# Kernel tuning notes

Measured on AMD Instinct MI355X. Metric: run time of the kernel, lower is better.

The kernel has to match this reference:

```python
import jax, jax.numpy as jnp
import numpy as np

BATCH = 8
N_CLASSES = 3            # including background
PRE_NMS_LIMIT = 6000
NMS_THRESH = 0.5
SCALE = 512.0
WINDOW = (0.0, 0.0, 512.0, 512.0)   # y1, x1, y2, x2
STD_DEV = np.array([0.1, 0.1, 0.2, 0.2], np.float32)
GROUP_OFFSET = 4096.0    # > image extent; separates (batch, class) groups in NMS

_RATIOS = np.array([0.5, 1.0, 2.0])
_LEVELS = [((128, 128), 4, 8.0), ((64, 64), 8, 16.0), ((32, 32), 16, 32.0), ((16, 16), 32, 64.0)]


def _gen_anchors():
    # faithful port of generate_pyramid_anchors / generate_anchors (anchor_stride=1)
    out = []
    for (fy, fx), stride, scale in _LEVELS:
        s, r = np.meshgrid(np.array([scale]), _RATIOS)
        s, r = s.flatten(), r.flatten()
        heights = s / np.sqrt(r)
        widths = s * np.sqrt(r)
        sy = np.arange(fy) * stride
        sx = np.arange(fx) * stride
        sx, sy = np.meshgrid(sx, sy)
        bw, bcx = np.meshgrid(widths, sx)
        bh, bcy = np.meshgrid(heights, sy)
        centers = np.stack([bcy, bcx], axis=2).reshape(-1, 2)
        sizes = np.stack([bh, bw], axis=2).reshape(-1, 2)
        out.append(np.concatenate([centers - 0.5 * sizes, centers + 0.5 * sizes], axis=1))
    return np.concatenate(out, axis=0).astype(np.float32)  # (65280, 4) yxyx


def setup_inputs() -> dict:
    key = jax.random.key(0)
    k1, k2 = jax.random.split(key)
    anchors = jnp.asarray(_gen_anchors())
    n_anchors = anchors.shape[0]
    n_prop = BATCH * n_anchors
    logits = jax.random.normal(k1, (n_prop, N_CLASSES), jnp.float32)
    probs = jax.nn.softmax(logits, axis=-1)
    deltas = jax.random.normal(k2, (n_prop, 4), jnp.float32)
    batch_ixs = jnp.repeat(jnp.arange(BATCH, dtype=jnp.int64), n_anchors)
    return {"probs": probs, "deltas": deltas, "anchors": anchors, "batch_ixs": batch_ixs}


def _apply_box_deltas_2d(boxes, deltas):
    # boxes: (K,4) yxyx (normalized); deltas: (K,4) dy,dx,dh,dw
    h = boxes[:, 2] - boxes[:, 0]
    w = boxes[:, 3] - boxes[:, 1]
    cy = boxes[:, 0] + 0.5 * h + deltas[:, 0] * h
    cx = boxes[:, 1] + 0.5 * w + deltas[:, 1] * w
    h = h * jnp.exp(deltas[:, 2])
    w = w * jnp.exp(deltas[:, 3])
    y1 = cy - 0.5 * h
    x1 = cx - 0.5 * w
    return jnp.stack([y1, x1, y1 + h, x1 + w], axis=1)


def _nms_keep(boxes, thresh):
    # boxes (K,4), already sorted by score descending; returns bool keep mask.
    y1, x1, y2, x2 = boxes[:, 0], boxes[:, 1], boxes[:, 2], boxes[:, 3]
    areas = (y2 - y1 + 1.0) * (x2 - x1 + 1.0)
    ih = jnp.clip(jnp.minimum(y2[:, None], y2[None, :]) - jnp.maximum(y1[:, None], y1[None, :]) + 1.0, 0.0)
    iw = jnp.clip(jnp.minimum(x2[:, None], x2[None, :]) - jnp.maximum(x1[:, None], x1[None, :]) + 1.0, 0.0)
    inter = ih * iw
    iou = inter / (areas[:, None] + areas[None, :] - inter)  # (K,K)
    K = boxes.shape[0]
    idx = jnp.arange(K)

    def body(i, keep):
        sup = (iou[i] >= thresh) & (idx > i) & keep[i]
        return keep & ~sup

    return jax.lax.fori_loop(0, K, body, jnp.ones((K,), bool))


def reference(probs, deltas, anchors, batch_ixs):
    n_anchors = anchors.shape[0]
    n_fg = probs.shape[1] - 1
    # trim to top pre_nms_limit foreground scores (flat over proposals x fg classes)
    fg = probs[:, 1:].reshape(-1)
    scores, flat_ix = jax.lax.top_k(fg, PRE_NMS_LIMIT)  # sorted descending
    prop_ix = flat_ix // n_fg
    class_ids = flat_ix % n_fg + 1
    b = batch_ixs[prop_ix]
    a = anchors[prop_ix % n_anchors]        # anchors tiled per batch element
    d = deltas[prop_ix] * jnp.asarray(STD_DEV)
    rois = _apply_box_deltas_2d(a / SCALE, d) * SCALE
    lo = jnp.array([WINDOW[0], WINDOW[1], WINDOW[0], WINDOW[1]], rois.dtype)
    hi = jnp.array([WINDOW[2], WINDOW[3], WINDOW[2], WINDOW[3]], rois.dtype)
    rois = jnp.clip(rois, lo, hi)
    # batched per-class NMS: offset boxes so different (batch, class) groups never overlap
    group = (b * (n_fg + 1) + class_ids).astype(rois.dtype) * GROUP_OFFSET
    keep = _nms_keep(rois + group[:, None], NMS_THRESH)
    detections = jnp.concatenate(
        [rois, scores[:, None], keep.astype(rois.dtype)[:, None]], axis=1)  # (K, 6)
    return detections, class_ids, b
```

## Files before the change

kernel.cpp:

```cpp
#include <hip/hip_runtime.h>
#include <math.h>

typedef unsigned int u32;
typedef unsigned short u16;
typedef unsigned long long u64;

#define PRE_NMS 6000
#define NBLK    94
#define KMAX    640
#define MSTRIDE 11
#define MAXW    10
#define MTILE   (MAXW * MAXW)
#define FINEB   8192
#define LOWB    8064
#define TOTB    (FINEB + LOWB)
#define NHB     32
#define CANDMAX 16384
#define NGRP    24
#define FLOOR_BITS 0x3F000000u

#define CTR_OFF    0
#define CAND_OFF   256
#define BOXR_OFF   131328
#define GBITS_OFF  227584
#define KG_OFF     246016
#define GRANKG_OFF 246272
#define BOXG_OFF   307712
#define AREAG_OFF  553472
#define MASKG_OFF  614912
#define BASE_OFF   1966592
#define BCNT_OFF   2032128
#define PART_OFF   2097664

__device__ __forceinline__ u32 bucket_of(u32 bits) {
    if (bits >= FLOOR_BITS) {
        u32 fb = (bits - FLOOR_BITS) >> 10; if (fb > FINEB - 1) fb = FINEB - 1;
        return fb;
    }
    return 8192u + (bits >> 17);
}

__global__ __launch_bounds__(1024) void hist_kernel(const float4* __restrict__ probs4,
                                                    u32* __restrict__ partials, int n_prop) {
    __shared__ u32 hf[FINEB];
    __shared__ u32 hl[2][LOWB];
    int t = threadIdx.x;
    for (int i = t; i < FINEB; i += 1024) hf[i] = 0u;
    for (int i = t; i < 2 * LOWB; i += 1024) ((u32*)hl)[i] = 0u;
    __syncthreads();
    u32* l = hl[(t >> 6) & 1];
    int nq = n_prop >> 2;
    int idx = blockIdx.x * 1024 + t;
    int stride = gridDim.x * 1024;
    for (int q = idx; q < nq; q += stride) {
        float4 a = probs4[3 * q + 0];
        float4 b = probs4[3 * q + 1];
        float4 c = probs4[3 * q + 2];
        float vs[8] = {a.y, a.z, b.x, b.y, b.w, c.x, c.z, c.w};
        #pragma unroll
        for (int e = 0; e < 8; ++e) {
            u32 bits = __float_as_uint(vs[e]);
            if (bits >= FLOOR_BITS) {
                u32 fb = (bits - FLOOR_BITS) >> 10; if (fb >= FINEB) fb = FINEB - 1;
                atomicAdd(&hf[fb], 1u);
            } else {
                atomicAdd(&l[bits >> 17], 1u);
            }
        }
    }
    __syncthreads();
    u32* outp = partials + blockIdx.x * TOTB;
    for (int b = t; b < FINEB; b += 1024) outp[b] = hf[b];
    for (int b = t; b < LOWB; b += 1024) outp[FINEB + b] = hl[0][b] + hl[1][b];
}

__global__ __launch_bounds__(1024) void pivot_kernel(const u32* __restrict__ partials,
                                                     u32* __restrict__ ctr,
                                                     u32* __restrict__ base,
                                                     u32* __restrict__ bcnt,
                                                     u32* __restrict__ gbits) {
    __shared__ u32 fh[FINEB];
    __shared__ u32 sd[1024];
    int t = threadIdx.x;
    for (int i = t; i < 16384; i += 1024) bcnt[i] = 0u;
    for (int i = t; i < NGRP * 192; i += 1024) gbits[i] = 0u;
    if (t == 0) { ctr[0] = 0u; ctr[1] = 0u; }
    for (int b = t; b < FINEB; b += 1024) {
        u32 s = 0;
        #pragma unroll
        for (int k = 0; k < NHB; ++k) s += partials[k * TOTB + b];
        fh[b] = s;
    }
    __syncthreads();
    int hi = FINEB - 1 - 8 * t;
    u32 L = 0;
    #pragma unroll
    for (int e = 0; e < 8; ++e) L += fh[hi - e];
    sd[t] = L;
    __syncthreads();
    for (int off = 1; off < 1024; off <<= 1) {
        u32 x = (t >= off) ? sd[t - off] : 0u;
        __syncthreads();
        sd[t] += x;
        __syncthreads();
    }
    u32 incl = sd[t], excl = incl - L;
    u32 fineTotal = sd[1023];
    {
        u32 run = excl;
        #pragma unroll
        for (int e = 0; e < 8; ++e) {
            int fb = hi - e;
            base[fb] = run;
            u32 c = fh[fb];
            if (run < (u32)PRE_NMS && run + c >= (u32)PRE_NMS) {
                ctr[1] = FLOOR_BITS + ((u32)fb << 10);
                u32 m = run + c; if (m > (u32)CANDMAX) m = (u32)CANDMAX;
                ctr[0] = m;
            }
            run += c;
        }
    }
    if (fineTotal >= (u32)PRE_NMS) return;

    u32 rem = (u32)PRE_NMS - fineTotal;
    __syncthreads();
    for (int b = t; b < FINEB; b += 1024) {
        u32 s = 0;
        if (b < LOWB) {
            #pragma unroll
            for (int k = 0; k < NHB; ++k) s += partials[k * TOTB + FINEB + b];
        }
        fh[b] = s;
    }
    __syncthreads();
    L = 0;
    #pragma unroll
    for (int e = 0; e < 8; ++e) L += fh[hi - e];
    sd[t] = L;
    __syncthreads();
    for (int off = 1; off < 1024; off <<= 1) {
        u32 x = (t >= off) ? sd[t - off] : 0u;
        __syncthreads();
        sd[t] += x;
        __syncthreads();
    }
    incl = sd[t]; excl = incl - L;
    {
        u32 run = excl;
        #pragma unroll
        for (int e = 0; e < 8; ++e) {
            int lb = hi - e;
            base[8192 + lb] = fineTotal + run;
            u32 c = fh[lb];
            if (run < rem && run + c >= rem) {
                ctr[1] = ((u32)lb) << 17;
                u32 m = fineTotal + run + c; if (m > (u32)CANDMAX) m = (u32)CANDMAX;
                ctr[0] = m;
            }
            run += c;
        }
    }
}

__global__ __launch_bounds__(256) void scatter_kernel(const float4* __restrict__ probs4,
                                                      const u32* __restrict__ ctr,
                                                      const u32* __restrict__ base,
                                                      u32* __restrict__ bcnt,
                                                      u64* __restrict__ cand,
                                                      int n_prop) {
    u32 pivot = ctr[1];
    int nq = n_prop >> 2;
    int idx = blockIdx.x * 256 + threadIdx.x;
    int stride = gridDim.x * 256;
    for (int q = idx; q < nq; q += stride) {
        float4 a = probs4[3 * q + 0];
        float4 b = probs4[3 * q + 1];
        float4 c = probs4[3 * q + 2];
        float vs[8] = {a.y, a.z, b.x, b.y, b.w, c.x, c.z, c.w};
        #pragma unroll
        for (int e = 0; e < 8; ++e) {
            u32 bits = __float_as_uint(vs[e]);
            if (bits >= pivot) {
                u32 bk = bucket_of(bits);
                u32 off = atomicAdd(&bcnt[bk], 1u);
                u32 slot = base[bk] + off;
                u32 i = (u32)(8 * q + e);
                if (slot < (u32)CANDMAX) cand[slot] = ((u64)bits << 32) | (u64)(~i);
            }
        }
    }
}

__global__ __launch_bounds__(256) void rankdecode_kernel(const u64* __restrict__ cand,
                                                         const u32* __restrict__ ctr,
                                                         const u32* __restrict__ base,
                                                         const u32* __restrict__ bcnt,
                                                         const float4* __restrict__ deltas4,
                                                         const float4* __restrict__ anchors4,
                                                         float4* __restrict__ boxr,
                                                         u32* __restrict__ gbits,
                                                         float* __restrict__ out,
                                                         int n_anch) {
    u32 M = ctr[0]; if (M > (u32)CANDMAX) M = (u32)CANDMAX;
    u32 i = blockIdx.x * 256 + threadIdx.x;
    if (i >= M) return;
    u64 key = cand[i];
    u32 bits = (u32)(key >> 32);
    u32 bk = bucket_of(bits);
    u32 b0 = base[bk];
    u32 n = bcnt[bk];
    u32 r = b0;
    if (n > 1) {
        u32 end = b0 + n; if (end > M) end = M;
        u32 cnt = 0;
        for (u32 j = b0; j < end; ++j) cnt += (cand[j] > key) ? 1u : 0u;
        r = b0 + cnt;
    }
    if (r >= (u32)PRE_NMS) return;
    u32 flat = ~((u32)key);
    int p = (int)(flat >> 1);
    int cls = (int)(flat & 1u) + 1;
    int b = p / n_anch;
    int g = b * 3 + cls;
    int aidx = p - b * n_anch;
    float score = __uint_as_float(bits);
    float4 a = anchors4[aidx];
    float4 d = deltas4[p];
    float d0 = d.x * 0.1f, d1 = d.y * 0.1f, d2 = d.z * 0.2f, d3 = d.w * 0.2f;
    float y1 = a.x * (1.0f / 512.0f), x1 = a.y * (1.0f / 512.0f);
    float y2 = a.z * (1.0f / 512.0f), x2 = a.w * (1.0f / 512.0f);
    float h = y2 - y1, w = x2 - x1;
    float cy = y1 + 0.5f * h + d0 * h;
    float cx = x1 + 0.5f * w + d1 * w;
    h = h * expf(d2);
    w = w * expf(d3);
    float ry1 = (cy - 0.5f * h) * 512.0f;
    float rx1 = (cx - 0.5f * w) * 512.0f;
    float ry2 = (cy - 0.5f * h + h) * 512.0f;
    float rx2 = (cx - 0.5f * w + w) * 512.0f;
    ry1 = fminf(fmaxf(ry1, 0.0f), 512.0f);
    rx1 = fminf(fmaxf(rx1, 0.0f), 512.0f);
    ry2 = fminf(fmaxf(ry2, 0.0f), 512.0f);
    rx2 = fminf(fmaxf(rx2, 0.0f), 512.0f);
    out[r * 6 + 0] = ry1;
    out[r * 6 + 1] = rx1;
    out[r * 6 + 2] = ry2;
    out[r * 6 + 3] = rx2;
    out[r * 6 + 4] = score;
    out[r * 6 + 5] = 1.0f;
    out[PRE_NMS * 6 + r] = (float)cls;
    out[PRE_NMS * 7 + r] = (float)b;
    boxr[r] = make_float4(ry1, rx1, ry2, rx2);
    atomicOr(&gbits[g * 192 + (r >> 5)], 1u << (r & 31));
}

__global__ __launch_bounds__(512) void prep_kernel(const u32* __restrict__ gbits,
                                                   const float4* __restrict__ boxr,
                                                   u32* __restrict__ kg,
                                                   u32* __restrict__ grankg,
                                                   float4* __restrict__ boxg,
                                                   float* __restrict__ areag) {
    __shared__ int bpre[96];
    __shared__ u16 grankS[KMAX];
    __shared__ int sK;
    int g = blockIdx.x, t = threadIdx.x, lane = t & 63, wv = t >> 6;
    const u32* rb32 = gbits + g * 192;

    if (t < 64) {
        u64 w0 = (u64)rb32[2 * lane] | ((u64)rb32[2 * lane + 1] << 32);
        u64 w1 = (lane < NBLK - 64)
                 ? ((u64)rb32[128 + 2 * lane] | ((u64)rb32[129 + 2 * lane] << 32)) : 0ull;
        int c0 = (int)__popcll(w0), c1 = (int)__popcll(w1);
        int i0 = c0, i1 = c1;
        #pragma unroll
        for (int off = 1; off < 64; off <<= 1) {
            int a = __shfl_up(i0, off); if (lane >= off) i0 += a;
            int b = __shfl_up(i1, off); if (lane >= off) i1 += b;
        }
        int tot0 = __shfl(i0, 63), tot1 = __shfl(i1, 63);
        bpre[lane] = i0 - c0;
        if (lane < 32) bpre[64 + lane] = tot0 + ((lane < NBLK - 64) ? (i1 - c1) : 0);
        if (lane == 0) { sK = tot0 + tot1; kg[g] = (u32)(tot0 + tot1); }
    }
    __syncthreads();
    int K = sK;
    if (K == 0) return;
    int Kc = (K < KMAX) ? K : KMAX;

    for (int blk = wv; blk < NBLK; blk += 8) {
        u64 wmask = (u64)rb32[2 * blk] | ((u64)rb32[2 * blk + 1] << 32);
        if ((wmask >> lane) & 1ull) {
            int pos = bpre[blk] + (int)__popcll(wmask & ((1ull << lane) - 1ull));
            if (pos < KMAX) grankS[pos] = (u16)((blk << 6) | lane);
        }
    }
    __syncthreads();

    float4* bg = boxg + g * KMAX;
    float*  ag = areag + g * KMAX;
    u32*    gr = grankg + g * KMAX;
    for (int m = t; m < KMAX; m += 512) {
        if (m < Kc) {
            int r = grankS[m];
            float4 bb = boxr[r];
            bg[m] = bb;
            ag[m] = (bb.z - bb.x + 1.0f) * (bb.w - bb.y + 1.0f);
            gr[m] = (u32)r;
        } else {
            bg[m] = make_float4(-3e30f, -3e30f, -3e30f, -3e30f);
            ag[m] = 3e38f;
        }
    }
}

__global__ __launch_bounds__(64) void mask_kernel(const u32* __restrict__ kg,
                                                  const float4* __restrict__ boxg,
                                                  const float* __restrict__ areag,
                                                  u64* __restrict__ maskg) {
    int g = blockIdx.y;
    u32 K = kg[g];
    if (K == 0u) return;
    int Kc = (K < (u32)KMAX) ? (int)K : KMAX;
    int W = (Kc + 63) >> 6;
    int u = blockIdx.x;
    int c = u / MAXW, rbk = u % MAXW;
    if (c >= W || rbk >= W) return;
    int lane = threadIdx.x;
    int r = rbk * 64 + lane;
    u64* mg = maskg + (size_t)g * (KMAX * MSTRIDE);
    if (rbk > c) { mg[r * MSTRIDE + c] = 0ull; return; }
    int j0 = c << 6;
    const float4* bg = boxg + g * KMAX;
    const float*  ag = areag + g * KMAX;
    float4 rb = bg[r];
    float  ra = ag[r];
    float4 cb = bg[j0 + lane];
    float  ca = ag[j0 + lane];
    u64 word = 0ull;
    #pragma unroll 8
    for (int q = 0; q < 64; ++q) {
        float cbx = __shfl(cb.x, q);
        float cby = __shfl(cb.y, q);
        float cbz = __shfl(cb.z, q);
        float cbw = __shfl(cb.w, q);
        float cav = __shfl(ca, q);
        float ih = fminf(rb.z, cbz) - fmaxf(rb.x, cbx) + 1.0f;
        float iw = fminf(rb.w, cbw) - fmaxf(rb.y, cby) + 1.0f;
        ih = fmaxf(ih, 0.0f); iw = fmaxf(iw, 0.0f);
        bool o = (3.0f * ih * iw >= ra + cav) && ((j0 + q) > r);
        if (o) word |= (1ull << q);
    }
    mg[r * MSTRIDE + c] = word;
}

__global__ __launch_bounds__(512) void greedy_kernel(const u32* __restrict__ kg,
                                                     const u32* __restrict__ grankg,
                                                     const u64* __restrict__ maskg,
                                                     float* __restrict__ out) {
    __shared__ u64 maskm[KMAX * MSTRIDE + 64];
    __shared__ u16 grank[KMAX];
    int g = blockIdx.x, t = threadIdx.x, lane = t & 63;
    u32 K = kg[g];
    if (K == 0u) return;
    int Kc = (K < (u32)KMAX) ? (int)K : KMAX;
    int W = (Kc + 63) >> 6;
    const u64* mg = maskg + (size_t)g * (KMAX * MSTRIDE);
    int nw = Kc * MSTRIDE;
    for (int m = t; m < nw; m += 512) maskm[m] = mg[m];
    for (int m = nw + t; m < nw + 64; m += 512) maskm[m] = 0ull;
    for (int m = t; m < Kc; m += 512) grank[m] = (u16)grankg[g * KMAX + m];
    __syncthreads();

    if (t >= 64) return;
    u64 remv = 0ull;
    for (int w = 0; w < W; ++w) {
        int r0 = w << 6;
        int rend = Kc - r0; if (rend > 64) rend = 64;
        u64 curw = __shfl(remv, w);
        u64 kb = 0ull;
        for (int b0 = 0; b0 < rend; b0 += 8) {
            int n = rend - b0; if (n > 8) n = 8;
            u64 mrow[8], dg[8];
            #pragma unroll
            for (int j = 0; j < 8; ++j) {
                int rr = r0 + b0 + ((j < n) ? j : 0);
                mrow[j] = maskm[rr * MSTRIDE + lane];
                dg[j]   = maskm[rr * MSTRIDE + w];
            }
            #pragma unroll
            for (int j = 0; j < 8; ++j) {
                if (j < n) {
                    int b = b0 + j;
                    u64 km = ((curw >> b) & 1ull) ? 0ull : ~0ull;
                    curw |= dg[j] & km;
                    remv |= mrow[j] & km;
                    kb |= km & (1ull << b);
                }
            }
        }
        if (lane < rend)
            out[(int)grank[r0 + lane] * 6 + 5] = ((kb >> lane) & 1ull) ? 1.0f : 0.0f;
    }
}

extern "C" void kernel_launch(void* const* d_in, const int* in_sizes, int n_in,
                              void* d_out, int out_size, void* d_ws, size_t ws_size,
                              hipStream_t stream) {
    const float*  probs    = (const float*)d_in[0];
    const float4* deltas4  = (const float4*)d_in[1];
    const float4* anchors4 = (const float4*)d_in[2];
    int n_prop = in_sizes[1] / 4;
    int n_anch = in_sizes[2] / 4;

    char* ws = (char*)d_ws;
    u32* ctr      = (u32*)(ws + CTR_OFF);
    u64* cand     = (u64*)(ws + CAND_OFF);
    float4* boxr  = (float4*)(ws + BOXR_OFF);
    u32* gbits    = (u32*)(ws + GBITS_OFF);
    u32* kg       = (u32*)(ws + KG_OFF);
    u32* grankg   = (u32*)(ws + GRANKG_OFF);
    float4* boxg  = (float4*)(ws + BOXG_OFF);
    float* areag  = (float*)(ws + AREAG_OFF);
    u64* maskg    = (u64*)(ws + MASKG_OFF);
    u32* base     = (u32*)(ws + BASE_OFF);
    u32* bcnt     = (u32*)(ws + BCNT_OFF);
    u32* partials = (u32*)(ws + PART_OFF);
    float* out    = (float*)d_out;

    hist_kernel<<<NHB, 1024, 0, stream>>>((const float4*)probs, partials, n_prop);
    pivot_kernel<<<1, 1024, 0, stream>>>(partials, ctr, base, bcnt, gbits);
    scatter_kernel<<<256, 256, 0, stream>>>((const float4*)probs, ctr, base, bcnt,
                                            cand, n_prop);
    rankdecode_kernel<<<CANDMAX / 256, 256, 0, stream>>>(cand, ctr, base, bcnt,
                                                         deltas4, anchors4,
                                                         boxr, gbits, out, n_anch);
    prep_kernel<<<NGRP, 512, 0, stream>>>(gbits, boxr, kg, grankg, boxg, areag);
    mask_kernel<<<dim3(MTILE, NGRP), 64, 0, stream>>>(kg, boxg, areag, maskg);
    greedy_kernel<<<NGRP, 512, 0, stream>>>(kg, grankg, maskg, out);
}
```

Baseline: 171.4 us.

## Merge fine histograms with global atomics and zero buffers via memset

Each histogram block now adds its non-zero fine-bucket counts atomically into one global histogram. Before, it wrote a full per-block copy that the single-block pivot kernel then summed, so the pivot kernel now reads one fine histogram instead of reducing all partials. The histogram grid doubles to 64 blocks, and zeroing of bcnt/gbits moves from the pivot kernel into a hipMemsetAsync before the histogram pass. The cost is an extra memset launch, global atomic contention, and a rarely taken low-bucket fallback that now sums 64 partials without unrolling.

```diff
diff --git a/kernel.cpp b/kernel.cpp
--- a/kernel.cpp
+++ b/kernel.cpp
@@ -13,24 +13,25 @@
 #define MTILE   (MAXW * MAXW)
 #define FINEB   8192
 #define LOWB    8064
-#define TOTB    (FINEB + LOWB)
-#define NHB     32
+#define NHB     64
 #define CANDMAX 16384
 #define NGRP    24
 #define FLOOR_BITS 0x3F000000u
 
 #define CTR_OFF    0
-#define CAND_OFF   256
-#define BOXR_OFF   131328
-#define GBITS_OFF  227584
-#define KG_OFF     246016
-#define GRANKG_OFF 246272
-#define BOXG_OFF   307712
-#define AREAG_OFF  553472
-#define MASKG_OFF  614912
-#define BASE_OFF   1966592
-#define BCNT_OFF   2032128
-#define PART_OFF   2097664
+#define FINEH_OFF  256
+#define BCNT_OFF   33024
+#define GBITS_OFF  98560
+#define ZERO_LEN   (32768 + 65536 + 18432)
+#define CAND_OFF   116992
+#define BOXR_OFF   248064
+#define KG_OFF     344320
+#define GRANKG_OFF 344576
+#define BOXG_OFF   406016
+#define AREAG_OFF  651776
+#define MASKG_OFF  713216
+#define BASE_OFF   2064896
+#define PART_OFF   2130432
 
 __device__ __forceinline__ u32 bucket_of(u32 bits) {
     if (bits >= FLOOR_BITS) {
@@ -41,6 +42,7 @@
 }
 
 __global__ __launch_bounds__(1024) void hist_kernel(const float4* __restrict__ probs4,
+                                                    u32* __restrict__ fineh,
                                                     u32* __restrict__ partials, int n_prop) {
     __shared__ u32 hf[FINEB];
     __shared__ u32 hl[2][LOWB];
@@ -69,28 +71,23 @@
         }
     }
     __syncthreads();
-    u32* outp = partials + blockIdx.x * TOTB;
-    for (int b = t; b < FINEB; b += 1024) outp[b] = hf[b];
-    for (int b = t; b < LOWB; b += 1024) outp[FINEB + b] = hl[0][b] + hl[1][b];
-}
-
-__global__ __launch_bounds__(1024) void pivot_kernel(const u32* __restrict__ partials,
+    for (int b = t; b < FINEB; b += 1024) {
+        u32 v = hf[b];
+        if (v) atomicAdd(&fineh[b], v);
+    }
+    u32* outp = partials + blockIdx.x * LOWB;
+    for (int b = t; b < LOWB; b += 1024) outp[b] = hl[0][b] + hl[1][b];
+}
+
+__global__ __launch_bounds__(1024) void pivot_kernel(const u32* __restrict__ fineh,
+                                                     const u32* __restrict__ partials,
                                                      u32* __restrict__ ctr,
-                                                     u32* __restrict__ base,
-                                                     u32* __restrict__ bcnt,
-                                                     u32* __restrict__ gbits) {
+                                                     u32* __restrict__ base) {
     __shared__ u32 fh[FINEB];
     __shared__ u32 sd[1024];
     int t = threadIdx.x;
-    for (int i = t; i < 16384; i += 1024) bcnt[i] = 0u;
-    for (int i = t; i < NGRP * 192; i += 1024) gbits[i] = 0u;
     if (t == 0) { ctr[0] = 0u; ctr[1] = 0u; }
-    for (int b = t; b < FINEB; b += 1024) {
-        u32 s = 0;
-        #pragma unroll
-        for (int k = 0; k < NHB; ++k) s += partials[k * TOTB + b];
-        fh[b] = s;
-    }
+    for (int b = t; b < FINEB; b += 1024) fh[b] = fineh[b];
     __syncthreads();
     int hi = FINEB - 1 - 8 * t;
     u32 L = 0;
@@ -128,8 +125,7 @@
     for (int b = t; b < FINEB; b += 1024) {
         u32 s = 0;
         if (b < LOWB) {
-            #pragma unroll
-            for (int k = 0; k < NHB; ++k) s += partials[k * TOTB + FINEB + b];
+            for (int k = 0; k < NHB; ++k) s += partials[k * LOWB + b];
         }
         fh[b] = s;
     }
@@ -415,21 +411,23 @@
 
     char* ws = (char*)d_ws;
     u32* ctr      = (u32*)(ws + CTR_OFF);
+    u32* fineh    = (u32*)(ws + FINEH_OFF);
+    u32* bcnt     = (u32*)(ws + BCNT_OFF);
+    u32* gbits    = (u32*)(ws + GBITS_OFF);
     u64* cand     = (u64*)(ws + CAND_OFF);
     float4* boxr  = (float4*)(ws + BOXR_OFF);
-    u32* gbits    = (u32*)(ws + GBITS_OFF);
     u32* kg       = (u32*)(ws + KG_OFF);
     u32* grankg   = (u32*)(ws + GRANKG_OFF);
     float4* boxg  = (float4*)(ws + BOXG_OFF);
     float* areag  = (float*)(ws + AREAG_OFF);
     u64* maskg    = (u64*)(ws + MASKG_OFF);
     u32* base     = (u32*)(ws + BASE_OFF);
-    u32* bcnt     = (u32*)(ws + BCNT_OFF);
     u32* partials = (u32*)(ws + PART_OFF);
     float* out    = (float*)d_out;
 
-    hist_kernel<<<NHB, 1024, 0, stream>>>((const float4*)probs, partials, n_prop);
-    pivot_kernel<<<1, 1024, 0, stream>>>(partials, ctr, base, bcnt, gbits);
+    hipMemsetAsync(ws + FINEH_OFF, 0, ZERO_LEN, stream);
+    hist_kernel<<<NHB, 1024, 0, stream>>>((const float4*)probs, fineh, partials, n_prop);
+    pivot_kernel<<<1, 1024, 0, stream>>>(fineh, partials, ctr, base);
     scatter_kernel<<<256, 256, 0, stream>>>((const float4*)probs, ctr, base, bcnt,
                                             cand, n_prop);
     rankdecode_kernel<<<CANDMAX / 256, 256, 0, stream>>>(cand, ctr, base, bcnt,
```

Result: faster. 140.1 us (-18.3%).
